# Performance work log

Measured on AMD Instinct MI355X. Metric: run time of the kernel, lower is better.

Reference implementation:

```python
import jax, jax.numpy as jnp
import numpy as np

# config constants
H = 2048          # hidden_size
I_MOE = 1408      # moe_intermediate_size
E = 8             # n_routed_experts
TOP_K = 2         # num_experts_per_tok
NG = 4            # n_group
TOPK_G = 2        # topk_group
SCALE = 2.5       # routed_scaling_factor
N_SHARED = 2      # n_shared_experts
I_SHARED = I_MOE * N_SHARED
B, S = 1, 2048


def setup_inputs() -> dict:
    key = jax.random.key(0)
    ks = jax.random.split(key, 9)
    sc = 0.02
    return {
        "x": jax.random.normal(ks[0], (B, S, H), dtype=jnp.float32),
        "router_weight": jax.random.normal(ks[1], (E, H), dtype=jnp.float32) * sc,
        "e_score_correction_bias": jnp.zeros((E,), dtype=jnp.float32),
        "gate_w": jax.random.normal(ks[2], (E, I_MOE, H), dtype=jnp.float32) * sc,
        "up_w": jax.random.normal(ks[3], (E, I_MOE, H), dtype=jnp.float32) * sc,
        "down_w": jax.random.normal(ks[4], (E, H, I_MOE), dtype=jnp.float32) * sc,
        "shared_gate_w": jax.random.normal(ks[5], (I_SHARED, H), dtype=jnp.float32) * sc,
        "shared_up_w": jax.random.normal(ks[6], (I_SHARED, H), dtype=jnp.float32) * sc,
        "shared_down_w": jax.random.normal(ks[7], (H, I_SHARED), dtype=jnp.float32) * sc,
    }


def _mlp(x, gw, uw, dw):
    # SwiGLU MLP: down( silu(gate(x)) * up(x) )
    return (jax.nn.silu(x @ gw.T) * (x @ uw.T)) @ dw.T


def _route(x2d, rw, bias):
    T = x2d.shape[0]
    logits = x2d.astype(jnp.float32) @ rw.astype(jnp.float32).T          # [T,E]
    scores = jax.nn.sigmoid(logits)                                       # [T,E]
    sfc = scores + bias[None, :]                                          # [T,E]
    # group scores: sum of top-2 per group
    grp = sfc.reshape(T, NG, E // NG)
    group_scores = jnp.sum(jax.lax.top_k(grp, 2)[0], axis=-1)             # [T,NG]
    grp_idx = jax.lax.top_k(group_scores, TOPK_G)[1]                      # [T,topk_group]
    group_mask = jnp.zeros((T, NG), jnp.float32).at[
        jnp.arange(T)[:, None], grp_idx].set(1.0)                         # [T,NG]
    score_mask = jnp.repeat(group_mask, E // NG, axis=1)                  # [T,E]
    masked = jnp.where(score_mask > 0, sfc, 0.0)
    topk_idx = jax.lax.top_k(masked, TOP_K)[1]                            # [T,K]
    topk_w = jnp.take_along_axis(scores, topk_idx, axis=1)                # [T,K]
    topk_w = topk_w / (jnp.sum(topk_w, axis=-1, keepdims=True) + 1e-20)   # norm_topk_prob
    return topk_idx, topk_w * SCALE


def reference(x, router_weight, e_score_correction_bias, gate_w, up_w, down_w,
              shared_gate_w, shared_up_w, shared_down_w):
    orig_shape = x.shape
    x2d = x.reshape(-1, H)                                                # [T,H]
    T = x2d.shape[0]
    topk_idx, topk_w = _route(x2d, router_weight, e_score_correction_bias)
    # per-token per-expert combine weights [T,E] (top-k indices are distinct per token)
    cw = jnp.zeros((T, E), jnp.float32).at[
        jnp.arange(T)[:, None], topk_idx].add(topk_w)

    def expert_body(acc, ws):
        gw, uw, dw, cwe = ws  # gw/uw:[I,H], dw:[H,I], cwe:[T]
        y = _mlp(x2d, gw, uw, dw)
        return acc + cwe[:, None] * y, None

    routed, _ = jax.lax.scan(expert_body, jnp.zeros_like(x2d),
                             (gate_w, up_w, down_w, cw.T))
    out = routed.reshape(orig_shape) + _mlp(x, shared_gate_w, shared_up_w, shared_down_w)
    return out
```

## Files before the change

### kernel.cpp

```cpp
#include <hip/hip_runtime.h>
#include <hip/hip_bf16.h>
#include <math.h>

#define H 2048
#define IMOE 1408
#define NEXP 8
#define T_TOK 2048
#define ISH 2816
#define SCALEF 2.5f

#define NT_GU_R (IMOE / 64)
#define NT_GU_S (ISH / 64)
#define NT_DN   (H / 128)
#define GU_GRID (39 * NT_GU_R + 16 * NT_GU_S)
#define DN_GRID (39 * NT_DN + 16 * NT_DN)

#define W8_GU  2883584
#define W8_SH  720896
#define GUW8   (2 * W8_GU + 2 * W8_SH)
#define DNW8   (W8_GU + W8_SH)

typedef __attribute__((ext_vector_type(8))) short short8;
typedef __attribute__((ext_vector_type(4))) short short4v;
typedef __attribute__((ext_vector_type(4))) float floatx4;

__device__ inline float b2f(short v) {
    unsigned int u = ((unsigned int)(unsigned short)v) << 16;
    float f; __builtin_memcpy(&f, &u, 4); return f;
}
__device__ inline short f2b(float f) {
    __hip_bfloat16 h = __float2bfloat16(f);
    short s; __builtin_memcpy(&s, &h, 2); return s;
}

__device__ __forceinline__ void async16(const short* g, short* l) {
    __builtin_amdgcn_global_load_lds(
        (const __attribute__((address_space(1))) unsigned*)g,
        (__attribute__((address_space(3))) unsigned*)l, 16, 0, 0);
}

__device__ __forceinline__ int xcd_map(int orig, int nwg) {
    int q = nwg >> 3, r = nwg & 7;
    int x = orig & 7, s = orig >> 3;
    int base = (x < r) ? x * (q + 1) : r * (q + 1) + (x - r) * q;
    return base + s;
}

__device__ __forceinline__ void cvt8(const float* s, short* d, size_t local) {
    floatx4 v0 = *(const floatx4*)(s + local * 8);
    floatx4 v1 = *(const floatx4*)(s + local * 8 + 4);
    short8 o = { f2b(v0.x), f2b(v0.y), f2b(v0.z), f2b(v0.w),
                 f2b(v1.x), f2b(v1.y), f2b(v1.z), f2b(v1.w) };
    *(short8*)(d + local * 8) = o;
}

__global__ __launch_bounds__(256) void route_conv_kernel(
    const float* __restrict__ x, const float* __restrict__ rw,
    const float* __restrict__ bias,
    float* __restrict__ pairW, int2* __restrict__ pickE, short* __restrict__ xb,
    const float* __restrict__ gw, const float* __restrict__ uw,
    const float* __restrict__ sgw, const float* __restrict__ suw,
    short* __restrict__ gwb, short* __restrict__ uwb,
    short* __restrict__ sgwb, short* __restrict__ suwb)
{
    if (blockIdx.x >= 512) {
        int u = (blockIdx.x - 512) * 256 + threadIdx.x;
        for (; u < GUW8; u += 2048 * 256) {
            const float* s; short* d; int local;
            if (u < W8_GU)               { s = gw;  d = gwb;  local = u; }
            else if (u < 2 * W8_GU)      { s = uw;  d = uwb;  local = u - W8_GU; }
            else if (u < 2 * W8_GU + W8_SH) { s = sgw; d = sgwb; local = u - 2 * W8_GU; }
            else                         { s = suw; d = suwb; local = u - 2 * W8_GU - W8_SH; }
            cvt8(s, d, (size_t)local);
        }
        return;
    }

    const int wid  = (blockIdx.x * 256 + threadIdx.x) >> 6;
    const int lane = threadIdx.x & 63;
    const float* xr = x + (size_t)wid * H;
    short* xbrow = xb + (size_t)wid * H;

    float acc[NEXP];
#pragma unroll
    for (int e = 0; e < NEXP; ++e) acc[e] = 0.f;

#pragma unroll
    for (int c = 0; c < 8; ++c) {
        int idx = (c * 64 + lane) * 4;
        floatx4 xv = *(const floatx4*)(xr + idx);
#pragma unroll
        for (int e = 0; e < NEXP; ++e) {
            floatx4 wv = *(const floatx4*)(rw + e * H + idx);
            acc[e] += xv.x * wv.x + xv.y * wv.y + xv.z * wv.z + xv.w * wv.w;
        }
        short4v o = { f2b(xv.x), f2b(xv.y), f2b(xv.z), f2b(xv.w) };
        *(short4v*)(xbrow + idx) = o;
    }
#pragma unroll
    for (int e = 0; e < NEXP; ++e)
        for (int off = 32; off; off >>= 1)
            acc[e] += __shfl_xor(acc[e], off, 64);

    if (lane == 0) {
        float s[NEXP], sfc[NEXP];
#pragma unroll
        for (int e = 0; e < NEXP; ++e) {
            s[e]   = 1.0f / (1.0f + expf(-acc[e]));
            sfc[e] = s[e] + bias[e];
        }
        float gs[4];
#pragma unroll
        for (int g = 0; g < 4; ++g) gs[g] = sfc[2 * g] + sfc[2 * g + 1];
        int g1 = 0;
        for (int g = 1; g < 4; ++g) if (gs[g] > gs[g1]) g1 = g;
        int g2 = -1;
        for (int g = 0; g < 4; ++g) {
            if (g == g1) continue;
            if (g2 < 0 || gs[g] > gs[g2]) g2 = g;
        }
        float msk[NEXP];
#pragma unroll
        for (int e = 0; e < NEXP; ++e) {
            int g = e >> 1;
            msk[e] = (g == g1 || g == g2) ? sfc[e] : 0.0f;
        }
        int e1 = 0;
        for (int e = 1; e < NEXP; ++e) if (msk[e] > msk[e1]) e1 = e;
        int e2 = -1;
        for (int e = 0; e < NEXP; ++e) {
            if (e == e1) continue;
            if (e2 < 0 || msk[e] > msk[e2]) e2 = e;
        }
        float w1 = s[e1], w2 = s[e2];
        float inv = SCALEF / (w1 + w2 + 1e-20f);
        pairW[2 * wid]     = w1 * inv;
        pairW[2 * wid + 1] = w2 * inv;
        int2 pk; pk.x = e1; pk.y = e2;
        pickE[wid] = pk;
    }
}

__global__ __launch_bounds__(256) void build_lists(
    const int2* __restrict__ pickE, int* __restrict__ cnt,
    int* __restrict__ tokList, int* __restrict__ slotList)
{
    const int e = blockIdx.x;
    const int tid = threadIdx.x;
    __shared__ int pre[256];
    const int t0 = tid * 8;
    int2 p[8];
#pragma unroll
    for (int j = 0; j < 8; ++j) p[j] = pickE[t0 + j];
    int cme = 0;
#pragma unroll
    for (int j = 0; j < 8; ++j) cme += (p[j].x == e || p[j].y == e) ? 1 : 0;
    pre[tid] = cme;
    __syncthreads();
    for (int off = 1; off < 256; off <<= 1) {
        int v = (tid >= off) ? pre[tid - off] : 0;
        __syncthreads();
        pre[tid] += v;
        __syncthreads();
    }
    int base = pre[tid] - cme;
#pragma unroll
    for (int j = 0; j < 8; ++j) {
        if (p[j].x == e || p[j].y == e) {
            tokList[e * T_TOK + base]  = t0 + j;
            slotList[e * T_TOK + base] = 2 * (t0 + j) + (p[j].x == e ? 0 : 1);
            ++base;
        }
    }
    if (tid == 255) cnt[e] = pre[255];
}

__global__ void plan_kernel(const int* __restrict__ cnt, int* __restrict__ meta)
{
    if (blockIdx.x != 0 || threadIdx.x != 0) return;
    int base = 0, gu = 0, dn = 0;
    meta[20] = 0; meta[32] = 0;
    for (int e = 0; e < NEXP; ++e) {
        int M = cnt[e];
        meta[e] = M;
        meta[9 + e] = base;
        base += M;
        int MT = (M + 127) >> 7;
        gu += MT * NT_GU_R;
        dn += MT * NT_DN;
        meta[21 + e] = gu;
        meta[33 + e] = dn;
    }
    meta[8]  = T_TOK;
    meta[17] = 0;
    meta[29] = gu + 16 * NT_GU_S;
    meta[41] = dn + 16 * NT_DN;
}

__global__ __launch_bounds__(256) void gu_gemm(
    const short* __restrict__ xb,
    const short* __restrict__ gwb, const short* __restrict__ uwb,
    const short* __restrict__ sgwb, const short* __restrict__ suwb,
    short* __restrict__ hiddenP, short* __restrict__ hiddenS,
    const int* __restrict__ tokList, const int* __restrict__ meta,
    const float* __restrict__ dw, const float* __restrict__ sdw,
    short* __restrict__ dwb, short* __restrict__ sdwb)
{
    const int total = meta[29];
    if (blockIdx.x >= total) {
        int rid = blockIdx.x - total;
        if (rid >= 512) return;
        int u = rid * 256 + threadIdx.x;
        for (; u < DNW8; u += 512 * 256) {
            if (u < W8_GU) cvt8(dw, dwb, (size_t)u);
            else           cvt8(sdw, sdwb, (size_t)(u - W8_GU));
        }
        return;
    }
    const int idx = xcd_map(blockIdx.x, total);
    int e = 0;
    while (e < 8 && idx >= meta[21 + e]) ++e;

    int M, NT, Nout, rowBase;
    const short *b1, *b2;
    const int* gat;
    short* outP;
    if (e < 8) {
        M = meta[e]; NT = NT_GU_R; Nout = IMOE; rowBase = meta[9 + e];
        b1 = gwb + (size_t)e * IMOE * H;
        b2 = uwb + (size_t)e * IMOE * H;
        gat = tokList + e * T_TOK;
        outP = hiddenP;
    } else {
        M = T_TOK; NT = NT_GU_S; Nout = ISH; rowBase = 0;
        b1 = sgwb; b2 = suwb; gat = nullptr; outP = hiddenS;
    }
    const int MT = (M + 127) >> 7;
    const int local = idx - meta[20 + e];
    const int mt = local % MT;
    const int nt = local / MT;

    __shared__ short As[128 * 64];
    __shared__ short Bgu[128 * 64];

    const int tid  = threadIdx.x;
    const int w    = tid >> 6;
    const int lane = tid & 63;
    const int quad = lane >> 4;
    const int l16  = lane & 15;
    const int wm = w >> 1, wn = w & 1;

    const int r8 = lane >> 3;
    const int cs = (lane & 7) ^ r8;
    const short* aSrc[4];
    const short* bSrc[4];
    short* ldsA[4];
    short* ldsB[4];
#pragma unroll
    for (int i = 0; i < 4; ++i) {
        int r = w * 32 + i * 8 + r8;
        int p = mt * 128 + r;
        int pos = p < M ? p : (M - 1);
        int arow = gat ? gat[pos] : pos;
        aSrc[i] = xb + (size_t)arow * H + cs * 8;
        ldsA[i] = As + (w * 32 + i * 8) * 64;
        const short* wsrc = (r < 64) ? (b1 + (size_t)(nt * 64 + r) * H)
                                     : (b2 + (size_t)(nt * 64 + r - 64) * H);
        bSrc[i] = wsrc + cs * 8;
        ldsB[i] = Bgu + (w * 32 + i * 8) * 64;
    }

    floatx4 accg[4][2] = {};
    floatx4 accu[4][2] = {};

    for (int k0 = 0; k0 < H; k0 += 64) {
#pragma unroll
        for (int i = 0; i < 4; ++i) async16(aSrc[i] + k0, ldsA[i]);
#pragma unroll
        for (int i = 0; i < 4; ++i) async16(bSrc[i] + k0, ldsB[i]);
        __syncthreads();
        const int sw = l16 & 7;
        short8 af[4], bgf[2], buf[2];
#pragma unroll
        for (int kk2 = 0; kk2 < 2; ++kk2) {
            const int c = kk2 * 4 + quad;
#pragma unroll
            for (int m = 0; m < 4; ++m)
                af[m] = *(const short8*)(As + (wm * 64 + m * 16 + l16) * 64 + (c ^ sw) * 8);
#pragma unroll
            for (int n = 0; n < 2; ++n) {
                bgf[n] = *(const short8*)(Bgu + (wn * 32 + n * 16 + l16) * 64 + (c ^ sw) * 8);
                buf[n] = *(const short8*)(Bgu + (64 + wn * 32 + n * 16 + l16) * 64 + (c ^ sw) * 8);
            }
#pragma unroll
            for (int m = 0; m < 4; ++m)
#pragma unroll
                for (int n = 0; n < 2; ++n) {
                    accg[m][n] = __builtin_amdgcn_mfma_f32_16x16x32_bf16(af[m], bgf[n], accg[m][n], 0, 0, 0);
                    accu[m][n] = __builtin_amdgcn_mfma_f32_16x16x32_bf16(af[m], buf[n], accu[m][n], 0, 0, 0);
                }
        }
        __syncthreads();
    }

#pragma unroll
    for (int m = 0; m < 4; ++m) {
#pragma unroll
        for (int rr = 0; rr < 4; ++rr) {
            int lr = wm * 64 + m * 16 + quad * 4 + rr;
            int p = mt * 128 + lr;
            if (p >= M) continue;
            size_t rowoff = (size_t)(rowBase + p) * Nout + nt * 64 + wn * 32;
#pragma unroll
            for (int n = 0; n < 2; ++n) {
                float g = accg[m][n][rr];
                float u = accu[m][n][rr];
                outP[rowoff + n * 16 + l16] = f2b(g / (1.0f + __expf(-g)) * u);
            }
        }
    }
}

__global__ __launch_bounds__(256) void dn_gemm(
    const short* __restrict__ hiddenP, const short* __restrict__ hiddenS,
    const short* __restrict__ dwb, const short* __restrict__ sdwb,
    short* __restrict__ outPairs, short* __restrict__ sharedOut,
    const int* __restrict__ slotList, const int* __restrict__ meta)
{
    const int total = meta[41];
    if (blockIdx.x >= total) return;
    const int rtot = meta[40];
    int idx;
    if (blockIdx.x < rtot) idx = xcd_map(blockIdx.x, rtot);
    else                   idx = rtot + xcd_map(blockIdx.x - rtot, total - rtot);
    int e = 0;
    while (e < 8 && idx >= meta[33 + e]) ++e;

    int M, K, rowBase;
    const short* bp;
    const short* Abase;
    const int* scat;
    short* outP;
    if (e < 8) {
        M = meta[e]; K = IMOE; rowBase = meta[9 + e];
        bp = dwb + (size_t)e * H * IMOE;
        Abase = hiddenP; scat = slotList + e * T_TOK; outP = outPairs;
    } else {
        M = T_TOK; K = ISH; rowBase = 0;
        bp = sdwb; Abase = hiddenS; scat = nullptr; outP = sharedOut;
    }
    const int MT = (M + 127) >> 7;
    const int local = idx - meta[32 + e];
    const int mt = local % MT;
    const int nt = local / MT;

    __shared__ short As[128 * 64];
    __shared__ short Bs[128 * 64];

    const int tid  = threadIdx.x;
    const int w    = tid >> 6;
    const int lane = tid & 63;
    const int quad = lane >> 4;
    const int l16  = lane & 15;
    const int wm = w >> 1, wn = w & 1;

    const int r8 = lane >> 3;
    const int cs = (lane & 7) ^ r8;
    const short* aSrc[4];
    const short* bSrc[4];
    short* ldsA[4];
    short* ldsB[4];
#pragma unroll
    for (int i = 0; i < 4; ++i) {
        int r = w * 32 + i * 8 + r8;
        int p = mt * 128 + r;
        int pos = p < M ? p : (M - 1);
        aSrc[i] = Abase + (size_t)(rowBase + pos) * K + cs * 8;
        ldsA[i] = As + (w * 32 + i * 8) * 64;
        bSrc[i] = bp + (size_t)(nt * 128 + r) * K + cs * 8;
        ldsB[i] = Bs + (w * 32 + i * 8) * 64;
    }

    floatx4 acc[4][4] = {};

    const int kIters = K >> 6;
    for (int kt = 0; kt < kIters; ++kt) {
        const int k0 = kt << 6;
#pragma unroll
        for (int i = 0; i < 4; ++i) async16(aSrc[i] + k0, ldsA[i]);
#pragma unroll
        for (int i = 0; i < 4; ++i) async16(bSrc[i] + k0, ldsB[i]);
        __syncthreads();
        const int sw = l16 & 7;
        short8 af[4], bf[4];
#pragma unroll
        for (int kk2 = 0; kk2 < 2; ++kk2) {
            const int c = kk2 * 4 + quad;
#pragma unroll
            for (int m = 0; m < 4; ++m)
                af[m] = *(const short8*)(As + (wm * 64 + m * 16 + l16) * 64 + (c ^ sw) * 8);
#pragma unroll
            for (int n = 0; n < 4; ++n)
                bf[n] = *(const short8*)(Bs + (wn * 64 + n * 16 + l16) * 64 + (c ^ sw) * 8);
#pragma unroll
            for (int m = 0; m < 4; ++m)
#pragma unroll
                for (int n = 0; n < 4; ++n)
                    acc[m][n] = __builtin_amdgcn_mfma_f32_16x16x32_bf16(af[m], bf[n], acc[m][n], 0, 0, 0);
        }
        __syncthreads();
    }

#pragma unroll
    for (int m = 0; m < 4; ++m) {
#pragma unroll
        for (int rr = 0; rr < 4; ++rr) {
            int lr = wm * 64 + m * 16 + quad * 4 + rr;
            int p = mt * 128 + lr;
            if (p >= M) continue;
            int crow = scat ? scat[p] : p;
            size_t rowoff = (size_t)crow * H + nt * 128 + wn * 64;
#pragma unroll
            for (int n = 0; n < 4; ++n)
                outP[rowoff + n * 16 + l16] = f2b(acc[m][n][rr]);
        }
    }
}

__global__ __launch_bounds__(256) void combine_kernel(
    const short* __restrict__ outPairs, const short* __restrict__ sharedOut,
    const float* __restrict__ pairW, float* __restrict__ out)
{
    size_t gi = ((size_t)blockIdx.x * 256 + threadIdx.x) * 8;
    int t = (int)(gi >> 11);
    int h = (int)(gi & (H - 1));
    float w0 = pairW[2 * t], w1 = pairW[2 * t + 1];
    short8 p0 = *(const short8*)(outPairs + (size_t)(2 * t) * H + h);
    short8 p1 = *(const short8*)(outPairs + (size_t)(2 * t + 1) * H + h);
    short8 sh = *(const short8*)(sharedOut + gi);
    floatx4 o0, o1;
#pragma unroll
    for (int j = 0; j < 4; ++j)
        o0[j] = w0 * b2f(p0[j]) + w1 * b2f(p1[j]) + b2f(sh[j]);
#pragma unroll
    for (int j = 0; j < 4; ++j)
        o1[j] = w0 * b2f(p0[4 + j]) + w1 * b2f(p1[4 + j]) + b2f(sh[4 + j]);
    *(floatx4*)(out + gi)     = o0;
    *(floatx4*)(out + gi + 4) = o1;
}

extern "C" void kernel_launch(void* const* d_in, const int* in_sizes, int n_in,
                              void* d_out, int out_size, void* d_ws, size_t ws_size,
                              hipStream_t stream)
{
    const float* x    = (const float*)d_in[0];
    const float* rw   = (const float*)d_in[1];
    const float* bias = (const float*)d_in[2];
    const float* gw   = (const float*)d_in[3];
    const float* uw   = (const float*)d_in[4];
    const float* dw   = (const float*)d_in[5];
    const float* sgw  = (const float*)d_in[6];
    const float* suw  = (const float*)d_in[7];
    const float* sdw  = (const float*)d_in[8];
    float* out = (float*)d_out;

    char* ws = (char*)d_ws;
    size_t off = 0;
    auto alloc = [&](size_t bytes) {
        off = (off + 255) & ~(size_t)255;
        void* p = ws + off;
        off += bytes;
        return p;
    };
    int*   cnt       = (int*)  alloc(NEXP * sizeof(int));
    int*   tokList   = (int*)  alloc((size_t)NEXP * T_TOK * sizeof(int));
    int*   slotList  = (int*)  alloc((size_t)NEXP * T_TOK * sizeof(int));
    float* pairW     = (float*)alloc((size_t)2 * T_TOK * sizeof(float));
    int2*  pickE     = (int2*) alloc((size_t)T_TOK * sizeof(int2));
    int*   meta      = (int*)  alloc(64 * sizeof(int));
    short* xb        = (short*)alloc((size_t)T_TOK * H * sizeof(short));
    short* hiddenP   = (short*)alloc((size_t)2 * T_TOK * IMOE * sizeof(short));
    short* hiddenS   = (short*)alloc((size_t)T_TOK * ISH * sizeof(short));
    short* outPairs  = (short*)alloc((size_t)2 * T_TOK * H * sizeof(short));
    short* sharedOut = (short*)alloc((size_t)T_TOK * H * sizeof(short));
    short* gwb  = (short*)alloc((size_t)NEXP * IMOE * H * sizeof(short));
    short* uwb  = (short*)alloc((size_t)NEXP * IMOE * H * sizeof(short));
    short* dwb  = (short*)alloc((size_t)NEXP * H * IMOE * sizeof(short));
    short* sgwb = (short*)alloc((size_t)ISH * H * sizeof(short));
    short* suwb = (short*)alloc((size_t)ISH * H * sizeof(short));
    short* sdwb = (short*)alloc((size_t)H * ISH * sizeof(short));
    (void)ws_size;

    route_conv_kernel<<<2560, 256, 0, stream>>>(x, rw, bias, pairW, pickE, xb,
                                                gw, uw, sgw, suw,
                                                gwb, uwb, sgwb, suwb);
    build_lists<<<NEXP, 256, 0, stream>>>(pickE, cnt, tokList, slotList);
    plan_kernel<<<1, 64, 0, stream>>>(cnt, meta);

    gu_gemm<<<GU_GRID + 512, 256, 0, stream>>>(xb, gwb, uwb, sgwb, suwb,
                                               hiddenP, hiddenS, tokList, meta,
                                               dw, sdw, dwb, sdwb);
    dn_gemm<<<DN_GRID, 256, 0, stream>>>(hiddenP, hiddenS, dwb, sdwb,
                                         outPairs, sharedOut, slotList, meta);

    combine_kernel<<<(T_TOK * H / 8) / 256, 256, 0, stream>>>(outPairs, sharedOut, pairW, out);
}
```

Baseline: 579.4 us.

## Double-buffer LDS tiles to prefetch next K-slice during MFMA compute

Both the gate/up and down GEMM kernels now allocate two LDS buffers per operand and issue async global-to-LDS loads for the next K tile before computing on the current one. This leaves one barrier per iteration and is meant to overlap global memory latency with MFMA work. It doubles LDS usage per block, which may reduce the number of resident blocks per CU.

```diff
diff --git a/kernel.cpp b/kernel.cpp
--- a/kernel.cpp
+++ b/kernel.cpp
@@ -14,6 +14,7 @@
 #define NT_DN   (H / 128)
 #define GU_GRID (39 * NT_GU_R + 16 * NT_GU_S)
 #define DN_GRID (39 * NT_DN + 16 * NT_DN)
+#define LHALF 8192
 
 #define W8_GU  2883584
 #define W8_SH  720896
@@ -240,8 +241,8 @@
     const int mt = local % MT;
     const int nt = local / MT;
 
-    __shared__ short As[128 * 64];
-    __shared__ short Bgu[128 * 64];
+    __shared__ short As[2 * LHALF];
+    __shared__ short Bgu[2 * LHALF];
 
     const int tid  = threadIdx.x;
     const int w    = tid >> 6;
@@ -273,12 +274,23 @@
     floatx4 accg[4][2] = {};
     floatx4 accu[4][2] = {};
 
+#pragma unroll
+    for (int i = 0; i < 4; ++i) { async16(aSrc[i], ldsA[i]); async16(bSrc[i], ldsB[i]); }
+    __syncthreads();
+
+    int cur = 0;
     for (int k0 = 0; k0 < H; k0 += 64) {
-#pragma unroll
-        for (int i = 0; i < 4; ++i) async16(aSrc[i] + k0, ldsA[i]);
-#pragma unroll
-        for (int i = 0; i < 4; ++i) async16(bSrc[i] + k0, ldsB[i]);
-        __syncthreads();
+        const int nk = k0 + 64;
+        const int noff = (cur ^ 1) * LHALF;
+        if (nk < H) {
+#pragma unroll
+            for (int i = 0; i < 4; ++i) {
+                async16(aSrc[i] + nk, ldsA[i] + noff);
+                async16(bSrc[i] + nk, ldsB[i] + noff);
+            }
+        }
+        const short* Ab = As  + cur * LHALF;
+        const short* Bb = Bgu + cur * LHALF;
         const int sw = l16 & 7;
         short8 af[4], bgf[2], buf[2];
 #pragma unroll
@@ -286,11 +298,11 @@
             const int c = kk2 * 4 + quad;
 #pragma unroll
             for (int m = 0; m < 4; ++m)
-                af[m] = *(const short8*)(As + (wm * 64 + m * 16 + l16) * 64 + (c ^ sw) * 8);
+                af[m] = *(const short8*)(Ab + (wm * 64 + m * 16 + l16) * 64 + (c ^ sw) * 8);
 #pragma unroll
             for (int n = 0; n < 2; ++n) {
-                bgf[n] = *(const short8*)(Bgu + (wn * 32 + n * 16 + l16) * 64 + (c ^ sw) * 8);
-                buf[n] = *(const short8*)(Bgu + (64 + wn * 32 + n * 16 + l16) * 64 + (c ^ sw) * 8);
+                bgf[n] = *(const short8*)(Bb + (wn * 32 + n * 16 + l16) * 64 + (c ^ sw) * 8);
+                buf[n] = *(const short8*)(Bb + (64 + wn * 32 + n * 16 + l16) * 64 + (c ^ sw) * 8);
             }
 #pragma unroll
             for (int m = 0; m < 4; ++m)
@@ -301,6 +313,7 @@
                 }
         }
         __syncthreads();
+        cur ^= 1;
     }
 
 #pragma unroll
@@ -354,8 +367,8 @@
     const int mt = local % MT;
     const int nt = local / MT;
 
-    __shared__ short As[128 * 64];
-    __shared__ short Bs[128 * 64];
+    __shared__ short As[2 * LHALF];
+    __shared__ short Bs[2 * LHALF];
 
     const int tid  = threadIdx.x;
     const int w    = tid >> 6;
@@ -383,14 +396,24 @@
 
     floatx4 acc[4][4] = {};
 
+#pragma unroll
+    for (int i = 0; i < 4; ++i) { async16(aSrc[i], ldsA[i]); async16(bSrc[i], ldsB[i]); }
+    __syncthreads();
+
     const int kIters = K >> 6;
+    int cur = 0;
     for (int kt = 0; kt < kIters; ++kt) {
-        const int k0 = kt << 6;
-#pragma unroll
-        for (int i = 0; i < 4; ++i) async16(aSrc[i] + k0, ldsA[i]);
-#pragma unroll
-        for (int i = 0; i < 4; ++i) async16(bSrc[i] + k0, ldsB[i]);
-        __syncthreads();
+        const int nk = (kt + 1) << 6;
+        const int noff = (cur ^ 1) * LHALF;
+        if (kt + 1 < kIters) {
+#pragma unroll
+            for (int i = 0; i < 4; ++i) {
+                async16(aSrc[i] + nk, ldsA[i] + noff);
+                async16(bSrc[i] + nk, ldsB[i] + noff);
+            }
+        }
+        const short* Ab = As + cur * LHALF;
+        const short* Bb = Bs + cur * LHALF;
         const int sw = l16 & 7;
         short8 af[4], bf[4];
 #pragma unroll
@@ -398,10 +421,10 @@
             const int c = kk2 * 4 + quad;
 #pragma unroll
             for (int m = 0; m < 4; ++m)
-                af[m] = *(const short8*)(As + (wm * 64 + m * 16 + l16) * 64 + (c ^ sw) * 8);
+                af[m] = *(const short8*)(Ab + (wm * 64 + m * 16 + l16) * 64 + (c ^ sw) * 8);
 #pragma unroll
             for (int n = 0; n < 4; ++n)
-                bf[n] = *(const short8*)(Bs + (wn * 64 + n * 16 + l16) * 64 + (c ^ sw) * 8);
+                bf[n] = *(const short8*)(Bb + (wn * 64 + n * 16 + l16) * 64 + (c ^ sw) * 8);
 #pragma unroll
             for (int m = 0; m < 4; ++m)
 #pragma unroll
@@ -409,6 +432,7 @@
                     acc[m][n] = __builtin_amdgcn_mfma_f32_16x16x32_bf16(af[m], bf[n], acc[m][n], 0, 0, 0);
         }
         __syncthreads();
+        cur ^= 1;
     }
 
 #pragma unroll
```

New measurement: 583.4 us. About the same (+0.7%).
